# Kernel optimization log

Measured on AMD Instinct MI355X. Metric: run time of the kernel, lower is better.

## Reference

```python
import jax, jax.numpy as jnp
import numpy as np

B, L, M, D, H, FF, W = 2, 2048, 2048, 1024, 16, 4096, 64
DH = D // H


def _layernorm(x, g, b, eps=1e-5):
    mu = x.mean(-1, keepdims=True)
    var = ((x - mu) ** 2).mean(-1, keepdims=True)
    return (x - mu) / jnp.sqrt(var + eps) * g + b


def _mha(qx, kx, wq, bq, wk, bk, wv, bv, wo, bo, mask, bias):
    Bq, Lq, _ = qx.shape
    Lk = kx.shape[1]
    q = (qx @ wq + bq).reshape(Bq, Lq, H, DH).transpose(0, 2, 1, 3)  # [B,H,Lq,DH]
    k = (kx @ wk + bk).reshape(Bq, Lk, H, DH).transpose(0, 2, 1, 3)
    v = (kx @ wv + bv).reshape(Bq, Lk, H, DH).transpose(0, 2, 1, 3)
    s = jnp.einsum('bhqd,bhkd->bhqk', q, k) / jnp.sqrt(jnp.asarray(DH, qx.dtype))
    if bias is not None:
        s = s + bias[None]  # bias: [H,Lq,Lk]
    if mask is not None:
        s = jnp.where(mask[None, None], s, jnp.asarray(-1e9, qx.dtype))
    a = jax.nn.softmax(s, axis=-1)
    o = jnp.einsum('bhqk,bhkd->bhqd', a, v).transpose(0, 2, 1, 3).reshape(Bq, Lq, D)
    return o @ wo + bo


def _forward(x, mem,
             swq, sbq, swk, sbk, swv, sbv, swo, sbo,
             cwq, cbq, cwk, cbk, cwv, cbv, cwo, cbo,
             w1, b1, w2, b2,
             g1, be1, g2, be2, g3, be3):
    i = jnp.arange(L)[:, None]
    j = jnp.arange(L)[None, :]
    # causal local window mask: attend to j<=i with i-j < W
    mask = (j <= i) & ((i - j) < W)
    # ALiBi slopes for power-of-2 head counts: 2^{-8h/H}, h=1..H
    slopes = (2.0 ** (-8.0 * jnp.arange(1, H + 1, dtype=x.dtype) / H))
    bias = slopes[:, None, None] * (j - i).astype(x.dtype)[None]  # [H,L,L], <=0 on causal part
    sa = _mha(x, x, swq, sbq, swk, sbk, swv, sbv, swo, sbo, mask, bias)
    x = _layernorm(x + sa, g1, be1)
    # cross-attn mask is all ones -> no masking, no bias
    ca = _mha(x, mem, cwq, cbq, cwk, cbk, cwv, cbv, cwo, cbo, None, None)
    x = _layernorm(x + ca, g2, be2)
    ff = jax.nn.gelu(x @ w1 + b1, approximate=False) @ w2 + b2
    return _layernorm(x + ff, g3, be3)


def setup_inputs() -> dict:
    key = jax.random.key(0)
    ks = jax.random.split(key, 16)
    s = 0.02
    inp = {
        'x': jax.random.normal(ks[0], (B, L, D), jnp.float32),
        'mem': jax.random.normal(ks[1], (B, M, D), jnp.float32),
    }
    # self-attn params
    for n, k in zip(['swq', 'swk', 'swv', 'swo'], jax.random.split(ks[2], 4)):
        inp[n] = jax.random.normal(k, (D, D), jnp.float32) * s
    for n in ['sbq', 'sbk', 'sbv', 'sbo']:
        inp[n] = jnp.zeros((D,), jnp.float32)
    # cross-attn params
    for n, k in zip(['cwq', 'cwk', 'cwv', 'cwo'], jax.random.split(ks[3], 4)):
        inp[n] = jax.random.normal(k, (D, D), jnp.float32) * s
    for n in ['cbq', 'cbk', 'cbv', 'cbo']:
        inp[n] = jnp.zeros((D,), jnp.float32)
    # FFN params
    inp['w1'] = jax.random.normal(ks[4], (D, FF), jnp.float32) * s
    inp['b1'] = jnp.zeros((FF,), jnp.float32)
    inp['w2'] = jax.random.normal(ks[5], (FF, D), jnp.float32) * s
    inp['b2'] = jnp.zeros((D,), jnp.float32)
    # LayerNorm params
    for n in ['g1', 'g2', 'g3']:
        inp[n] = jnp.ones((D,), jnp.float32)
    for n in ['be1', 'be2', 'be3']:
        inp[n] = jnp.zeros((D,), jnp.float32)
    return inp


def reference(x, mem,
              swq, sbq, swk, sbk, swv, sbv, swo, sbo,
              cwq, cbq, cwk, cbk, cwv, cbv, cwo, cbo,
              w1, b1, w2, b2,
              g1, be1, g2, be2, g3, be3):
    return _forward(x, mem,
                    swq, sbq, swk, sbk, swv, sbv, swo, sbo,
                    cwq, cbq, cwk, cbk, cwv, cbv, cwo, cbo,
                    w1, b1, w2, b2,
                    g1, be1, g2, be2, g3, be3)
```

## Files before the change

kernel.cpp:

```cpp
#include <hip/hip_runtime.h>
#include <hip/hip_bf16.h>
#include <math.h>

#define Bc 2
#define Lc 2048
#define Mc 2048
#define Dc 1024
#define Hc 16
#define FFc 4096
#define DHc 64

typedef __bf16 bf16;
typedef float f32x4 __attribute__((ext_vector_type(4)));
typedef __bf16 bf16x8 __attribute__((ext_vector_type(8)));
typedef __bf16 bf16x4 __attribute__((ext_vector_type(4)));
typedef __bf16 bf16x2 __attribute__((ext_vector_type(2)));

struct Ptrs8 { const float* p[8]; };

__device__ inline void gload16(const bf16* g, const bf16* lds_base) {
  __builtin_amdgcn_global_load_lds(
      (const __attribute__((address_space(1))) void*)g,
      (__attribute__((address_space(3))) void*)lds_base, 16, 0, 0);
}

#define WAIT_VM(n) asm volatile("s_waitcnt vmcnt(" #n ")" ::: "memory")
#define WAIT_LGKM(n) asm volatile("s_waitcnt lgkmcnt(" #n ")" ::: "memory")
#define RAW_BAR() __builtin_amdgcn_s_barrier()
#define SCHED_FENCE() __builtin_amdgcn_sched_barrier(0)

__device__ inline float gelu_f(float v) {
  float u = 0.7978845608f * (v + 0.044715f * v * v * v);
  float e = exp2f(u * 2.885390082f);
  float th = 1.0f - 2.0f / (e + 1.0f);
  return 0.5f * v * (1.0f + th);
}

__device__ inline int xcd_remap(int flat, int nwg) {
  int cpx = nwg >> 3;
  return (flat & 7) * cpx + (flat >> 3);
}

__global__ __launch_bounds__(256) void k_f2b(const float* __restrict__ in,
                                             bf16* __restrict__ out, long n4) {
  long i = (long)blockIdx.x * 256 + threadIdx.x;
  if (i >= n4) return;
  f32x4 v = *(const f32x4*)(in + i * 4);
  bf16x4 o;
  o[0] = (bf16)v[0]; o[1] = (bf16)v[1]; o[2] = (bf16)v[2]; o[3] = (bf16)v[3];
  *(bf16x4*)(out + i * 4) = o;
}

__global__ __launch_bounds__(256) void k_transpose_w8(Ptrs8 srcs,
                                                      bf16* __restrict__ out) {
  __shared__ float tile[64][65];
  const float* in = srcs.p[blockIdx.z];
  bf16* o = out + (long)blockIdx.z * Dc * Dc;
  int n0 = blockIdx.x * 64, k0 = blockIdx.y * 64;
  int t = threadIdx.x;
  int tr = t >> 4, tc = (t & 15) * 4;
#pragma unroll
  for (int p = 0; p < 4; p++) {
    int r = p * 16 + tr;
    f32x4 v = *(const f32x4*)(in + (long)(k0 + r) * Dc + n0 + tc);
    tile[r][tc] = v[0]; tile[r][tc + 1] = v[1];
    tile[r][tc + 2] = v[2]; tile[r][tc + 3] = v[3];
  }
  __syncthreads();
#pragma unroll
  for (int p = 0; p < 4; p++) {
    int rn = p * 16 + tr;
    bf16x4 ov;
    ov[0] = (bf16)tile[tc + 0][rn]; ov[1] = (bf16)tile[tc + 1][rn];
    ov[2] = (bf16)tile[tc + 2][rn]; ov[3] = (bf16)tile[tc + 3][rn];
    *(bf16x4*)(o + (long)(n0 + rn) * Dc + k0 + tc) = ov;
  }
}

__global__ __launch_bounds__(256) void k_transpose_w(const float* __restrict__ in,
                                                     bf16* __restrict__ out,
                                                     int K, int N) {
  __shared__ float tile[64][65];
  int n0 = blockIdx.x * 64, k0 = blockIdx.y * 64;
  int t = threadIdx.x;
  int tr = t >> 4, tc = (t & 15) * 4;
#pragma unroll
  for (int p = 0; p < 4; p++) {
    int r = p * 16 + tr;
    f32x4 v = *(const f32x4*)(in + (long)(k0 + r) * N + n0 + tc);
    tile[r][tc] = v[0]; tile[r][tc + 1] = v[1];
    tile[r][tc + 2] = v[2]; tile[r][tc + 3] = v[3];
  }
  __syncthreads();
#pragma unroll
  for (int p = 0; p < 4; p++) {
    int rn = p * 16 + tr;
    bf16x4 o;
    o[0] = (bf16)tile[tc + 0][rn]; o[1] = (bf16)tile[tc + 1][rn];
    o[2] = (bf16)tile[tc + 2][rn]; o[3] = (bf16)tile[tc + 3][rn];
    *(bf16x4*)(out + (long)(n0 + rn) * K + k0 + tc) = o;
  }
}

__global__ __launch_bounds__(256) void k_transpose_v(const bf16* __restrict__ vb,
                                                     bf16* __restrict__ vt, int N) {
  __shared__ bf16 tile[64][72];
  int j0 = blockIdx.x * 64;
  int bh = blockIdx.y; int b = bh >> 4; int h = bh & 15;
  int t = threadIdx.x;
#pragma unroll
  for (int c = 0; c < 2; c++) {
    int id = t + c * 256;
    int r = id >> 3, c8 = (id & 7) * 8;
    *(bf16x8*)&tile[r][c8] =
        *(const bf16x8*)(vb + ((long)(b * N + j0 + r)) * Dc + h * DHc + c8);
  }
  __syncthreads();
#pragma unroll
  for (int c = 0; c < 2; c++) {
    int id = t + c * 256;
    int d = id >> 3, j8 = (id & 7) * 8;
    bf16x8 o;
#pragma unroll
    for (int e = 0; e < 8; e++) o[e] = tile[j8 + e][d];
    *(bf16x8*)(vt + ((long)bh * DHc + d) * N + j0 + j8) = o;
  }
}

__global__ __launch_bounds__(256) void k_gemm128(
    const bf16* __restrict__ A0, const bf16* __restrict__ A1,
    const bf16* __restrict__ A2, long lda,
    const bf16* __restrict__ B0, long bstride,
    bf16* __restrict__ outB, long ldc, long cstride,
    const float* __restrict__ bias0, const float* __restrict__ bias1,
    const float* __restrict__ bias2, int Kdim, int act, float scale0) {
  __shared__ __align__(16) bf16 As[2][128 * 64];
  __shared__ __align__(16) bf16 Bs[2][128 * 64];
  int gx = gridDim.x, gy = gridDim.y;
  int nwg = gx * gy * gridDim.z;
  int flat = (blockIdx.z * gy + blockIdx.y) * gx + blockIdx.x;
  int f2 = xcd_remap(flat, nwg);
  int bxi = f2 % gx; int tmp = f2 / gx;
  int byi = tmp % gy; int z = tmp / gy;
  const bf16* A = (z == 0) ? A0 : ((z == 1) ? A1 : A2);
  const bf16* Bt = B0 + (long)z * bstride;
  const float* bias = (z == 0) ? bias0 : ((z == 1) ? bias1 : bias2);
  float scl = (z == 0) ? scale0 : 1.0f;
  long cbase = (long)z * cstride;
  int bm = byi * 128, bn = bxi * 128;
  int t = threadIdx.x, w = t >> 6, lane = t & 63;
  int wm = w >> 1, wn = w & 1;
  int lr = lane & 15, lg = lane >> 4;
  int srow = lane >> 3;
  int scol = (((lane & 7) * 16) ^ ((lane >> 3) << 4)) >> 1;
  f32x4 acc[4][4] = {};
  int nk = Kdim >> 6;
  auto stage = [&](int buf, int kt2) {
    long k0 = (long)kt2 * 64;
#pragma unroll
    for (int i = 0; i < 4; i++) {
      int row = (i * 4 + w) * 8 + srow;
      gload16(A + (long)(bm + row) * lda + k0 + scol, &As[buf][(i * 4 + w) * 512]);
      gload16(Bt + (long)(bn + row) * Kdim + k0 + scol, &Bs[buf][(i * 4 + w) * 512]);
    }
  };
  stage(0, 0);
  if (nk > 1) stage(1, 1);
  for (int kt = 0; kt < nk; ++kt) {
    int cur = kt & 1;
    if (kt + 1 < nk) { WAIT_VM(8); } else { WAIT_VM(0); }
    RAW_BAR();
    SCHED_FENCE();
    const char* pa = (const char*)&As[cur][0];
    const char* pb = (const char*)&Bs[cur][0];
    int xr = (lr & 7) << 4;
    bf16x8 af[2][4], bfr[2][4];
#pragma unroll
    for (int m = 0; m < 4; m++) {
      int row = wm * 64 + m * 16 + lr;
      af[0][m] = *(const bf16x8*)(pa + (row << 7) + ((lg * 16) ^ xr));
    }
#pragma unroll
    for (int n = 0; n < 4; n++) {
      int row = wn * 64 + n * 16 + lr;
      bfr[0][n] = *(const bf16x8*)(pb + (row << 7) + ((lg * 16) ^ xr));
    }
    SCHED_FENCE();
#pragma unroll
    for (int m = 0; m < 4; m++) {
      int row = wm * 64 + m * 16 + lr;
      af[1][m] = *(const bf16x8*)(pa + (row << 7) + ((64 + lg * 16) ^ xr));
    }
#pragma unroll
    for (int n = 0; n < 4; n++) {
      int row = wn * 64 + n * 16 + lr;
      bfr[1][n] = *(const bf16x8*)(pb + (row << 7) + ((64 + lg * 16) ^ xr));
    }
    SCHED_FENCE();
    WAIT_LGKM(8);
    SCHED_FENCE();
#pragma unroll
    for (int m = 0; m < 4; m++)
#pragma unroll
      for (int n = 0; n < 4; n++)
        acc[m][n] = __builtin_amdgcn_mfma_f32_16x16x32_bf16(af[0][m], bfr[0][n],
                                                            acc[m][n], 0, 0, 0);
    WAIT_LGKM(0);
    SCHED_FENCE();
    RAW_BAR();
    if (kt + 2 < nk) stage(cur, kt + 2);
    SCHED_FENCE();
#pragma unroll
    for (int m = 0; m < 4; m++)
#pragma unroll
      for (int n = 0; n < 4; n++)
        acc[m][n] = __builtin_amdgcn_mfma_f32_16x16x32_bf16(af[1][m], bfr[1][n],
                                                            acc[m][n], 0, 0, 0);
  }
#pragma unroll
  for (int n = 0; n < 4; n++) {
    int cg = bn + wn * 64 + n * 16 + lr;
    float bv = bias ? bias[cg] : 0.0f;
#pragma unroll
    for (int m = 0; m < 4; m++) {
#pragma unroll
      for (int rr = 0; rr < 4; rr++) {
        int rg = bm + wm * 64 + m * 16 + lg * 4 + rr;
        float v = (acc[m][n][rr] + bv) * scl;
        if (act == 1) v = gelu_f(v);
        outB[cbase + (long)rg * ldc + cg] = (bf16)v;
      }
    }
  }
}

__global__ __launch_bounds__(256) void k_gemmsk(
    const bf16* __restrict__ A, long lda,
    const bf16* __restrict__ Bt, int Kfull,
    bf16* __restrict__ psum, long slab, int Kchunk, int ldc) {
  __shared__ __align__(16) bf16 As[2][128 * 64];
  __shared__ __align__(16) bf16 Bs[2][128 * 64];
  int gx = gridDim.x, gy = gridDim.y;
  int nwg = gx * gy * gridDim.z;
  int flat = (blockIdx.z * gy + blockIdx.y) * gx + blockIdx.x;
  int f2 = xcd_remap(flat, nwg);
  int bxi = f2 % gx; int tmp = f2 / gx;
  int byi = tmp % gy; int z = tmp / gy;
  int bm = byi * 128, bn = bxi * 128;
  int t = threadIdx.x, w = t >> 6, lane = t & 63;
  int wm = w >> 1, wn = w & 1;
  int lr = lane & 15, lg = lane >> 4;
  int srow = lane >> 3;
  int scol = (((lane & 7) * 16) ^ ((lane >> 3) << 4)) >> 1;
  f32x4 acc[4][4] = {};
  int nk = Kchunk >> 6;
  long kstart = (long)z * Kchunk;
  auto stage = [&](int buf, int kt2) {
    long k0 = kstart + (long)kt2 * 64;
#pragma unroll
    for (int i = 0; i < 4; i++) {
      int row = (i * 4 + w) * 8 + srow;
      gload16(A + (long)(bm + row) * lda + k0 + scol, &As[buf][(i * 4 + w) * 512]);
      gload16(Bt + (long)(bn + row) * Kfull + k0 + scol, &Bs[buf][(i * 4 + w) * 512]);
    }
  };
  stage(0, 0);
  if (nk > 1) stage(1, 1);
  for (int kt = 0; kt < nk; ++kt) {
    int cur = kt & 1;
    if (kt + 1 < nk) { WAIT_VM(8); } else { WAIT_VM(0); }
    RAW_BAR();
    SCHED_FENCE();
    const char* pa = (const char*)&As[cur][0];
    const char* pb = (const char*)&Bs[cur][0];
    int xr = (lr & 7) << 4;
    bf16x8 af[2][4], bfr[2][4];
#pragma unroll
    for (int m = 0; m < 4; m++) {
      int row = wm * 64 + m * 16 + lr;
      af[0][m] = *(const bf16x8*)(pa + (row << 7) + ((lg * 16) ^ xr));
    }
#pragma unroll
    for (int n = 0; n < 4; n++) {
      int row = wn * 64 + n * 16 + lr;
      bfr[0][n] = *(const bf16x8*)(pb + (row << 7) + ((lg * 16) ^ xr));
    }
    SCHED_FENCE();
#pragma unroll
    for (int m = 0; m < 4; m++) {
      int row = wm * 64 + m * 16 + lr;
      af[1][m] = *(const bf16x8*)(pa + (row << 7) + ((64 + lg * 16) ^ xr));
    }
#pragma unroll
    for (int n = 0; n < 4; n++) {
      int row = wn * 64 + n * 16 + lr;
      bfr[1][n] = *(const bf16x8*)(pb + (row << 7) + ((64 + lg * 16) ^ xr));
    }
    SCHED_FENCE();
    WAIT_LGKM(8);
    SCHED_FENCE();
#pragma unroll
    for (int m = 0; m < 4; m++)
#pragma unroll
      for (int n = 0; n < 4; n++)
        acc[m][n] = __builtin_amdgcn_mfma_f32_16x16x32_bf16(af[0][m], bfr[0][n],
                                                            acc[m][n], 0, 0, 0);
    WAIT_LGKM(0);
    SCHED_FENCE();
    RAW_BAR();
    if (kt + 2 < nk) stage(cur, kt + 2);
    SCHED_FENCE();
#pragma unroll
    for (int m = 0; m < 4; m++)
#pragma unroll
      for (int n = 0; n < 4; n++)
        acc[m][n] = __builtin_amdgcn_mfma_f32_16x16x32_bf16(af[1][m], bfr[1][n],
                                                            acc[m][n], 0, 0, 0);
  }
  bf16* po = psum + (long)z * slab;
#pragma unroll
  for (int n = 0; n < 4; n++) {
    int cg = bn + wn * 64 + n * 16 + lr;
#pragma unroll
    for (int m = 0; m < 4; m++) {
#pragma unroll
      for (int rr = 0; rr < 4; rr++) {
        int rg = bm + wm * 64 + m * 16 + lg * 4 + rr;
        po[(long)rg * ldc + cg] = (bf16)acc[m][n][rr];
      }
    }
  }
}

template <int WINDOWED>
__global__ __launch_bounds__(256) void k_flash(const bf16* __restrict__ Qg,
                                               const bf16* __restrict__ Kg,
                                               const bf16* __restrict__ Vtg,
                                               bf16* __restrict__ Og, int nkv) {
  __shared__ __align__(16) bf16 Qs[64 * 64];
  __shared__ __align__(16) bf16 Ks[2][64 * 64];
  __shared__ __align__(16) bf16 Vs[2][64 * 64];
  int flat = blockIdx.y * 32 + blockIdx.x;
  int flat2 = (flat & 7) * 128 + (flat >> 3);
  int i0 = (flat2 & 31) * 64;
  int bh = flat2 >> 5;
  int b = bh >> 4, h = bh & 15;
  int t = threadIdx.x, w = t >> 6, lane = t & 63;
  int lr = lane & 15, lg = lane >> 4;
  long qoff = ((long)b * Lc + i0) * Dc + h * DHc;
  long koff = ((long)b * nkv) * Dc + h * DHc;
  long vtoff = (long)bh * DHc * nkv;
  int o0 = w * 1024 + (lane << 4), o1 = o0 + 4096;
  int r0 = o0 >> 7, c0 = (o0 & 127) ^ ((r0 & 7) << 4);
  int r1 = o1 >> 7, c1 = (o1 & 127) ^ ((r1 & 7) << 4);
  int d0 = c0 >> 1, d1 = c1 >> 1;
  gload16(Qg + qoff + (long)r0 * Dc + d0, &Qs[w * 512]);
  gload16(Qg + qoff + (long)r1 * Dc + d1, &Qs[2048 + w * 512]);
  int kb0 = WINDOWED ? (i0 >= 64 ? i0 - 64 : 0) : 0;
  int nt = WINDOWED ? ((i0 - kb0) >> 6) + 1 : (nkv >> 6);
  auto stage = [&](int buf, int kbase) {
    gload16(Kg + koff + (long)(kbase + r0) * Dc + d0, &Ks[buf][w * 512]);
    gload16(Kg + koff + (long)(kbase + r1) * Dc + d1, &Ks[buf][2048 + w * 512]);
    gload16(Vtg + vtoff + (long)r0 * nkv + kbase + d0, &Vs[buf][w * 512]);
    gload16(Vtg + vtoff + (long)r1 * nkv + kbase + d1, &Vs[buf][2048 + w * 512]);
  };
  stage(0, kb0);
  WAIT_VM(4);
  RAW_BAR();
  SCHED_FENCE();
  bf16x8 bq[2];
#pragma unroll
  for (int ks = 0; ks < 2; ks++) {
    int rq = w * 16 + lr, cb = ks * 64 + lg * 16;
    bq[ks] = *(const bf16x8*)&Qs[((rq << 7) + (cb ^ ((rq & 7) << 4))) >> 1];
  }
  char* pbase = (char*)&Qs[w * 1024];
  float mrun = -1e30f, lrun = 0.f;
  float mx_c = 0.0f;
  f32x4 oa[4] = {};
  f32x4 lacc = {};
  bf16x8 ones;
#pragma unroll
  for (int e = 0; e < 8; e++) ones[e] = (bf16)1.0f;
  float slopeL2 = WINDOWED ? exp2f(-0.5f * (float)(h + 1)) * 1.44269504f : 0.0f;
  int qabs = i0 + w * 16 + lr;
  int xr16 = (lr & 7) << 4;
  for (int tch = 0; tch < nt; tch++) {
    int cur = tch & 1;
    if (tch + 1 < nt) {
      stage(cur ^ 1, kb0 + (tch + 1) * 64);
      WAIT_VM(4);
    } else {
      WAIT_VM(0);
    }
    RAW_BAR();
    SCHED_FENCE();
    int kbase = kb0 + tch * 64;
    f32x4 st[4] = {};
    __builtin_amdgcn_s_setprio(1);
#pragma unroll
    for (int ks = 0; ks < 2; ks++) {
#pragma unroll
      for (int m = 0; m < 4; m++) {
        int rk = m * 16 + lr, cb = ks * 64 + lg * 16;
        bf16x8 ka = *(const bf16x8*)&Ks[cur][((rk << 7) + (cb ^ ((rk & 7) << 4))) >> 1];
        st[m] = __builtin_amdgcn_mfma_f32_16x16x32_bf16(ka, bq[ks], st[m], 0, 0, 0);
      }
    }
    __builtin_amdgcn_s_setprio(0);
    if (WINDOWED) {
      float sc[4][4];
#pragma unroll
      for (int m = 0; m < 4; m++)
#pragma unroll
        for (int rr = 0; rr < 4; rr++) {
          float v = st[m][rr];
          int kab = kbase + m * 16 + lg * 4 + rr;
          v += slopeL2 * (float)(kab - qabs);
          bool valid = (kab <= qabs) && (qabs - kab < 64);
          sc[m][rr] = valid ? v : -3.0e38f;
        }
      float pmax = sc[0][0];
#pragma unroll
      for (int m = 0; m < 4; m++)
#pragma unroll
        for (int rr = 0; rr < 4; rr++) pmax = fmaxf(pmax, sc[m][rr]);
      pmax = fmaxf(pmax, __shfl_xor(pmax, 16));
      pmax = fmaxf(pmax, __shfl_xor(pmax, 32));
      float mx = mrun;
      if (!__all(pmax - mrun <= 8.0f)) {
        mx = fmaxf(mrun, pmax);
        float corr = exp2f(mrun - mx);
        mrun = mx;
        lrun *= corr;
        float cq[4];
#pragma unroll
        for (int rr = 0; rr < 4; rr++) cq[rr] = __shfl(corr, lg * 4 + rr);
#pragma unroll
        for (int jd = 0; jd < 4; jd++) {
          oa[jd][0] *= cq[0]; oa[jd][1] *= cq[1];
          oa[jd][2] *= cq[2]; oa[jd][3] *= cq[3];
        }
      }
      float ps = 0.f;
#pragma unroll
      for (int m = 0; m < 4; m++) {
        float p0 = exp2f(sc[m][0] - mx);
        float p1 = exp2f(sc[m][1] - mx);
        float p2 = exp2f(sc[m][2] - mx);
        float p3 = exp2f(sc[m][3] - mx);
        ps += (p0 + p1) + (p2 + p3);
        bf16x4 pw; pw[0] = (bf16)p0; pw[1] = (bf16)p1;
        pw[2] = (bf16)p2; pw[3] = (bf16)p3;
        *(bf16x4*)(pbase + (lr << 7) + ((m * 32 + lg * 8) ^ xr16)) = pw;
      }
      lrun += ps;
      __builtin_amdgcn_s_setprio(1);
#pragma unroll
      for (int ks = 0; ks < 2; ks++) {
        bf16x8 pa = *(const bf16x8*)(pbase + (lr << 7) +
                                     ((ks * 64 + lg * 16) ^ xr16));
#pragma unroll
        for (int jd = 0; jd < 4; jd++) {
          int rv = jd * 16 + lr, cb = ks * 64 + lg * 16;
          bf16x8 vf = *(const bf16x8*)&Vs[cur][((rv << 7) + (cb ^ ((rv & 7) << 4))) >> 1];
          oa[jd] = __builtin_amdgcn_mfma_f32_16x16x32_bf16(pa, vf, oa[jd], 0, 0, 0);
        }
      }
      __builtin_amdgcn_s_setprio(0);
    } else {
      if (tch == 0) {
        float pmax = st[0][0];
#pragma unroll
        for (int m = 0; m < 4; m++)
#pragma unroll
          for (int rr = 0; rr < 4; rr++) pmax = fmaxf(pmax, st[m][rr]);
        pmax = fmaxf(pmax, __shfl_xor(pmax, 16));
        pmax = fmaxf(pmax, __shfl_xor(pmax, 32));
        mx_c = pmax;
      }
#pragma unroll
      for (int m = 0; m < 4; m++) {
        float p0 = exp2f(st[m][0] - mx_c);
        float p1 = exp2f(st[m][1] - mx_c);
        float p2 = exp2f(st[m][2] - mx_c);
        float p3 = exp2f(st[m][3] - mx_c);
        bf16x4 pw; pw[0] = (bf16)p0; pw[1] = (bf16)p1;
        pw[2] = (bf16)p2; pw[3] = (bf16)p3;
        *(bf16x4*)(pbase + (lr << 7) + ((m * 32 + lg * 8) ^ xr16)) = pw;
      }
      __builtin_amdgcn_s_setprio(1);
#pragma unroll
      for (int ks = 0; ks < 2; ks++) {
        bf16x8 pa = *(const bf16x8*)(pbase + (lr << 7) +
                                     ((ks * 64 + lg * 16) ^ xr16));
        lacc = __builtin_amdgcn_mfma_f32_16x16x32_bf16(pa, ones, lacc, 0, 0, 0);
#pragma unroll
        for (int jd = 0; jd < 4; jd++) {
          int rv = jd * 16 + lr, cb = ks * 64 + lg * 16;
          bf16x8 vf = *(const bf16x8*)&Vs[cur][((rv << 7) + (cb ^ ((rv & 7) << 4))) >> 1];
          oa[jd] = __builtin_amdgcn_mfma_f32_16x16x32_bf16(pa, vf, oa[jd], 0, 0, 0);
        }
      }
      __builtin_amdgcn_s_setprio(0);
      float lm = fmaxf(fmaxf(lacc[0], lacc[1]), fmaxf(lacc[2], lacc[3]));
      if (!__all(lm < 16777216.0f)) {
        const float cs = 2.3283064365386963e-10f;
        mx_c += 32.0f;
#pragma unroll
        for (int jd = 0; jd < 4; jd++) {
          oa[jd][0] *= cs; oa[jd][1] *= cs;
          oa[jd][2] *= cs; oa[jd][3] *= cs;
        }
        lacc[0] *= cs; lacc[1] *= cs; lacc[2] *= cs; lacc[3] *= cs;
      }
    }
    WAIT_LGKM(0);
    SCHED_FENCE();
    RAW_BAR();
  }
  if (WINDOWED) {
    float ls = lrun + __shfl_xor(lrun, 16);
    ls += __shfl_xor(ls, 32);
    float inv = 1.0f / ls;
    float iq[4];
#pragma unroll
    for (int rr = 0; rr < 4; rr++) iq[rr] = __shfl(inv, lg * 4 + rr);
#pragma unroll
    for (int rr = 0; rr < 4; rr++) {
      int qo = i0 + w * 16 + lg * 4 + rr;
#pragma unroll
      for (int jd = 0; jd < 4; jd++)
        Og[((long)b * Lc + qo) * Dc + h * DHc + jd * 16 + lr] =
            (bf16)(oa[jd][rr] * iq[rr]);
    }
  } else {
#pragma unroll
    for (int rr = 0; rr < 4; rr++) {
      float inv = 1.0f / lacc[rr];
      int qo = i0 + w * 16 + lg * 4 + rr;
#pragma unroll
      for (int jd = 0; jd < 4; jd++)
        Og[((long)b * Lc + qo) * Dc + h * DHc + jd * 16 + lr] =
            (bf16)(oa[jd][rr] * inv);
    }
  }
}

template <int NS>
__global__ __launch_bounds__(256) void k_lnred(const bf16* __restrict__ psum,
                                               long slab,
                                               const float* __restrict__ bias,
                                               const float* __restrict__ addsrc,
                                               const float* __restrict__ g,
                                               const float* __restrict__ bb,
                                               float* __restrict__ outF,
                                               bf16* __restrict__ outB) {
  long row = blockIdx.x;
  int t = threadIdx.x; int lane = t & 63; int wid = t >> 6;
  __shared__ float red[8];
  bf16x4 v0 = *(const bf16x4*)(psum + row * Dc + t * 4);
  float v[4] = {(float)v0[0], (float)v0[1], (float)v0[2], (float)v0[3]};
#pragma unroll
  for (int s = 1; s < NS; s++) {
    bf16x4 u = *(const bf16x4*)(psum + s * slab + row * Dc + t * 4);
    v[0] += (float)u[0]; v[1] += (float)u[1];
    v[2] += (float)u[2]; v[3] += (float)u[3];
  }
  f32x4 bv = *(const f32x4*)(bias + t * 4);
  f32x4 av = *(const f32x4*)(addsrc + row * Dc + t * 4);
  v[0] += bv[0] + av[0]; v[1] += bv[1] + av[1];
  v[2] += bv[2] + av[2]; v[3] += bv[3] + av[3];
  float s = v[0] + v[1] + v[2] + v[3];
  float s2 = v[0] * v[0] + v[1] * v[1] + v[2] * v[2] + v[3] * v[3];
#pragma unroll
  for (int off = 1; off < 64; off <<= 1) {
    s += __shfl_xor(s, off);
    s2 += __shfl_xor(s2, off);
  }
  if (lane == 0) { red[wid] = s; red[4 + wid] = s2; }
  __syncthreads();
  s = red[0] + red[1] + red[2] + red[3];
  s2 = red[4] + red[5] + red[6] + red[7];
  float mu = s * (1.0f / Dc);
  float var = s2 * (1.0f / Dc) - mu * mu;
  float rs = rsqrtf(var + 1e-5f);
#pragma unroll
  for (int e = 0; e < 4; e++) {
    int c = t * 4 + e;
    float y = (v[e] - mu) * rs * g[c] + bb[c];
    if (outF) outF[row * Dc + c] = y;
    if (outB) outB[row * Dc + c] = (bf16)y;
  }
}

extern "C" void kernel_launch(void* const* d_in, const int* in_sizes, int n_in,
                              void* d_out, int out_size, void* d_ws,
                              size_t ws_size, hipStream_t stream) {
  (void)in_sizes; (void)n_in; (void)out_size; (void)ws_size;
  const float* x = (const float*)d_in[0];
  const float* mem = (const float*)d_in[1];
  const float* swq = (const float*)d_in[2];
  const float* swk = (const float*)d_in[3];
  const float* swv = (const float*)d_in[4];
  const float* swo = (const float*)d_in[5];
  const float* sbq = (const float*)d_in[6];
  const float* sbk = (const float*)d_in[7];
  const float* sbv = (const float*)d_in[8];
  const float* sbo = (const float*)d_in[9];
  const float* cwq = (const float*)d_in[10];
  const float* cwk = (const float*)d_in[11];
  const float* cwv = (const float*)d_in[12];
  const float* cwo = (const float*)d_in[13];
  const float* cbq = (const float*)d_in[14];
  const float* cbk = (const float*)d_in[15];
  const float* cbv = (const float*)d_in[16];
  const float* cbo = (const float*)d_in[17];
  const float* w1 = (const float*)d_in[18];
  const float* b1 = (const float*)d_in[19];
  const float* w2 = (const float*)d_in[20];
  const float* b2 = (const float*)d_in[21];
  const float* g1 = (const float*)d_in[22];
  const float* g2 = (const float*)d_in[23];
  const float* g3 = (const float*)d_in[24];
  const float* be1 = (const float*)d_in[25];
  const float* be2 = (const float*)d_in[26];
  const float* be3 = (const float*)d_in[27];
  float* out = (float*)d_out;

  char* ws = (char*)d_ws;
  size_t off = 0;
  auto alloc = [&](size_t bytes) -> char* {
    char* p = ws + off;
    off = (off + bytes + 255) & ~(size_t)255;
    return p;
  };

  const long BL = (long)Bc * Lc;
  const long BM = (long)Bc * Mc;
  const long DD = (long)Dc * Dc;
  const long SL = BL * Dc;
  const float QSCL = 0.125f * 1.44269504f;

  bf16* wT0 = (bf16*)alloc((size_t)8 * DD * 2);
  bf16* w1T = (bf16*)alloc((size_t)FFc * Dc * 2);
  bf16* w2T = (bf16*)alloc((size_t)Dc * FFc * 2);
  bf16* xb = (bf16*)alloc((size_t)BL * Dc * 2);
  bf16* memb = (bf16*)alloc((size_t)BM * Dc * 2);
  bf16* x1b = (bf16*)alloc((size_t)BL * Dc * 2);
  bf16* x2b = (bf16*)alloc((size_t)BL * Dc * 2);
  bf16* qb = (bf16*)alloc((size_t)BL * Dc * 2);
  bf16* kb = (bf16*)alloc((size_t)BM * Dc * 2);
  bf16* vb = (bf16*)alloc((size_t)BM * Dc * 2);
  bf16* ob = (bf16*)alloc((size_t)BL * Dc * 2);
  bf16* vtS = (bf16*)alloc((size_t)Bc * Hc * DHc * Lc * 2);
  bf16* vtC = (bf16*)alloc((size_t)Bc * Hc * DHc * Mc * 2);
  float* x1f = (float*)alloc((size_t)BL * Dc * 4);
  float* x2f = (float*)alloc((size_t)BL * Dc * 4);
  bf16* ffh = (bf16*)alloc((size_t)BL * FFc * 2);
  bf16* psum = (bf16*)alloc((size_t)4 * SL * 2);

  Ptrs8 srcs;
  srcs.p[0] = swq; srcs.p[1] = swk; srcs.p[2] = swv; srcs.p[3] = swo;
  srcs.p[4] = cwq; srcs.p[5] = cwk; srcs.p[6] = cwv; srcs.p[7] = cwo;
  k_transpose_w8<<<dim3(Dc / 64, Dc / 64, 8), 256, 0, stream>>>(srcs, wT0);
  k_transpose_w<<<dim3(FFc / 64, Dc / 64), 256, 0, stream>>>(w1, w1T, Dc, FFc);
  k_transpose_w<<<dim3(Dc / 64, FFc / 64), 256, 0, stream>>>(w2, w2T, FFc, Dc);
  k_f2b<<<dim3((unsigned)(BL * Dc / 4 / 256)), 256, 0, stream>>>(x, xb, BL * Dc / 4);
  k_f2b<<<dim3((unsigned)(BM * Dc / 4 / 256)), 256, 0, stream>>>(mem, memb, BM * Dc / 4);

  k_gemm128<<<dim3(Dc / 128, BL / 128, 3), 256, 0, stream>>>(
      xb, xb, xb, Dc, wT0, DD, qb, Dc, SL, sbq, sbk, sbv, Dc, 0, QSCL);
  k_transpose_v<<<dim3(Lc / 64, Bc * Hc), 256, 0, stream>>>(vb, vtS, Lc);
  k_flash<1><<<dim3(Lc / 64, Bc * Hc), 256, 0, stream>>>(qb, kb, vtS, ob, Lc);
  k_gemmsk<<<dim3(Dc / 128, BL / 128, 2), 256, 0, stream>>>(
      ob, Dc, wT0 + 3 * DD, Dc, psum, SL, 512, Dc);
  k_lnred<2><<<dim3((unsigned)BL), 256, 0, stream>>>(psum, SL, sbo, x, g1, be1,
                                                     x1f, x1b);

  k_gemm128<<<dim3(Dc / 128, BM / 128, 3), 256, 0, stream>>>(
      x1b, memb, memb, Dc, wT0 + 4 * DD, DD, qb, Dc, SL, cbq, cbk, cbv, Dc, 0, QSCL);
  k_transpose_v<<<dim3(Mc / 64, Bc * Hc), 256, 0, stream>>>(vb, vtC, Mc);
  k_flash<0><<<dim3(Lc / 64, Bc * Hc), 256, 0, stream>>>(qb, kb, vtC, ob, Mc);
  k_gemmsk<<<dim3(Dc / 128, BL / 128, 2), 256, 0, stream>>>(
      ob, Dc, wT0 + 7 * DD, Dc, psum, SL, 512, Dc);
  k_lnred<2><<<dim3((unsigned)BL), 256, 0, stream>>>(psum, SL, cbo, x1f, g2, be2,
                                                     x2f, x2b);

  k_gemm128<<<dim3(FFc / 128, BL / 128, 1), 256, 0, stream>>>(
      x2b, x2b, x2b, Dc, w1T, 0, ffh, FFc, 0, b1, b1, b1, Dc, 1, 1.0f);
  k_gemmsk<<<dim3(Dc / 128, BL / 128, 4), 256, 0, stream>>>(
      ffh, FFc, w2T, FFc, psum, SL, 1024, Dc);
  k_lnred<4><<<dim3((unsigned)BL), 256, 0, stream>>>(psum, SL, b2, x2f, g3, be3,
                                                     out, nullptr);
}
```

Measured before the change: 359.9 us.

## Split flash kernel; cross-attention processes 128 queries per block, add MFMA priority in GEMMs

The templated flash kernel is split into a self-attention version and a cross-attention version. The cross-attention kernel now handles 128 query rows per workgroup, 32 per wave, so each K/V tile staged into shared memory is reused by twice as many queries, halving K/V global traffic and the grid size. The Q buffer is reused as the per-wave P scratch. Separately, the GEMM kernels raise wave priority around the MFMA blocks. The trade-offs are more registers per wave, which may lower occupancy, and fewer workgroups to fill the GPU.

Result: no change. 363.6 us, median of 2 (+1.0%).

```diff
diff --git a/kernel.cpp b/kernel.cpp
--- a/kernel.cpp
+++ b/kernel.cpp
@@ -199,23 +199,27 @@
     SCHED_FENCE();
     WAIT_LGKM(8);
     SCHED_FENCE();
+    __builtin_amdgcn_s_setprio(1);
 #pragma unroll
     for (int m = 0; m < 4; m++)
 #pragma unroll
       for (int n = 0; n < 4; n++)
         acc[m][n] = __builtin_amdgcn_mfma_f32_16x16x32_bf16(af[0][m], bfr[0][n],
                                                             acc[m][n], 0, 0, 0);
+    __builtin_amdgcn_s_setprio(0);
     WAIT_LGKM(0);
     SCHED_FENCE();
     RAW_BAR();
     if (kt + 2 < nk) stage(cur, kt + 2);
     SCHED_FENCE();
+    __builtin_amdgcn_s_setprio(1);
 #pragma unroll
     for (int m = 0; m < 4; m++)
 #pragma unroll
       for (int n = 0; n < 4; n++)
         acc[m][n] = __builtin_amdgcn_mfma_f32_16x16x32_bf16(af[1][m], bfr[1][n],
                                                             acc[m][n], 0, 0, 0);
+    __builtin_amdgcn_s_setprio(0);
   }
 #pragma unroll
   for (int n = 0; n < 4; n++) {
@@ -299,23 +303,27 @@
     SCHED_FENCE();
     WAIT_LGKM(8);
     SCHED_FENCE();
+    __builtin_amdgcn_s_setprio(1);
 #pragma unroll
     for (int m = 0; m < 4; m++)
 #pragma unroll
       for (int n = 0; n < 4; n++)
         acc[m][n] = __builtin_amdgcn_mfma_f32_16x16x32_bf16(af[0][m], bfr[0][n],
                                                             acc[m][n], 0, 0, 0);
+    __builtin_amdgcn_s_setprio(0);
     WAIT_LGKM(0);
     SCHED_FENCE();
     RAW_BAR();
     if (kt + 2 < nk) stage(cur, kt + 2);
     SCHED_FENCE();
+    __builtin_amdgcn_s_setprio(1);
 #pragma unroll
     for (int m = 0; m < 4; m++)
 #pragma unroll
       for (int n = 0; n < 4; n++)
         acc[m][n] = __builtin_amdgcn_mfma_f32_16x16x32_bf16(af[1][m], bfr[1][n],
                                                             acc[m][n], 0, 0, 0);
+    __builtin_amdgcn_s_setprio(0);
   }
   bf16* po = psum + (long)z * slab;
 #pragma unroll
@@ -332,11 +340,10 @@
   }
 }
 
-template <int WINDOWED>
-__global__ __launch_bounds__(256) void k_flash(const bf16* __restrict__ Qg,
-                                               const bf16* __restrict__ Kg,
-                                               const bf16* __restrict__ Vtg,
-                                               bf16* __restrict__ Og, int nkv) {
+__global__ __launch_bounds__(256) void k_flash_self(const bf16* __restrict__ Qg,
+                                                    const bf16* __restrict__ Kg,
+                                                    const bf16* __restrict__ Vtg,
+                                                    bf16* __restrict__ Og, int nkv) {
   __shared__ __align__(16) bf16 Qs[64 * 64];
   __shared__ __align__(16) bf16 Ks[2][64 * 64];
   __shared__ __align__(16) bf16 Vs[2][64 * 64];
@@ -356,8 +363,8 @@
   int d0 = c0 >> 1, d1 = c1 >> 1;
   gload16(Qg + qoff + (long)r0 * Dc + d0, &Qs[w * 512]);
   gload16(Qg + qoff + (long)r1 * Dc + d1, &Qs[2048 + w * 512]);
-  int kb0 = WINDOWED ? (i0 >= 64 ? i0 - 64 : 0) : 0;
-  int nt = WINDOWED ? ((i0 - kb0) >> 6) + 1 : (nkv >> 6);
+  int kb0 = i0 >= 64 ? i0 - 64 : 0;
+  int nt = ((i0 - kb0) >> 6) + 1;
   auto stage = [&](int buf, int kbase) {
     gload16(Kg + koff + (long)(kbase + r0) * Dc + d0, &Ks[buf][w * 512]);
     gload16(Kg + koff + (long)(kbase + r1) * Dc + d1, &Ks[buf][2048 + w * 512]);
@@ -376,13 +383,8 @@
   }
   char* pbase = (char*)&Qs[w * 1024];
   float mrun = -1e30f, lrun = 0.f;
-  float mx_c = 0.0f;
   f32x4 oa[4] = {};
-  f32x4 lacc = {};
-  bf16x8 ones;
-#pragma unroll
-  for (int e = 0; e < 8; e++) ones[e] = (bf16)1.0f;
-  float slopeL2 = WINDOWED ? exp2f(-0.5f * (float)(h + 1)) * 1.44269504f : 0.0f;
+  float slopeL2 = exp2f(-0.5f * (float)(h + 1)) * 1.44269504f;
   int qabs = i0 + w * 16 + lr;
   int xr16 = (lr & 7) << 4;
   for (int tch = 0; tch < nt; tch++) {
@@ -408,143 +410,241 @@
       }
     }
     __builtin_amdgcn_s_setprio(0);
-    if (WINDOWED) {
-      float sc[4][4];
-#pragma unroll
-      for (int m = 0; m < 4; m++)
-#pragma unroll
-        for (int rr = 0; rr < 4; rr++) {
-          float v = st[m][rr];
-          int kab = kbase + m * 16 + lg * 4 + rr;
-          v += slopeL2 * (float)(kab - qabs);
-          bool valid = (kab <= qabs) && (qabs - kab < 64);
-          sc[m][rr] = valid ? v : -3.0e38f;
-        }
-      float pmax = sc[0][0];
-#pragma unroll
-      for (int m = 0; m < 4; m++)
-#pragma unroll
-        for (int rr = 0; rr < 4; rr++) pmax = fmaxf(pmax, sc[m][rr]);
+    float sc[4][4];
+#pragma unroll
+    for (int m = 0; m < 4; m++)
+#pragma unroll
+      for (int rr = 0; rr < 4; rr++) {
+        float v = st[m][rr];
+        int kab = kbase + m * 16 + lg * 4 + rr;
+        v += slopeL2 * (float)(kab - qabs);
+        bool valid = (kab <= qabs) && (qabs - kab < 64);
+        sc[m][rr] = valid ? v : -3.0e38f;
+      }
+    float pmax = sc[0][0];
+#pragma unroll
+    for (int m = 0; m < 4; m++)
+#pragma unroll
+      for (int rr = 0; rr < 4; rr++) pmax = fmaxf(pmax, sc[m][rr]);
+    pmax = fmaxf(pmax, __shfl_xor(pmax, 16));
+    pmax = fmaxf(pmax, __shfl_xor(pmax, 32));
+    float mx = mrun;
+    if (!__all(pmax - mrun <= 8.0f)) {
+      mx = fmaxf(mrun, pmax);
+      float corr = exp2f(mrun - mx);
+      mrun = mx;
+      lrun *= corr;
+      float cq[4];
+#pragma unroll
+      for (int rr = 0; rr < 4; rr++) cq[rr] = __shfl(corr, lg * 4 + rr);
+#pragma unroll
+      for (int jd = 0; jd < 4; jd++) {
+        oa[jd][0] *= cq[0]; oa[jd][1] *= cq[1];
+        oa[jd][2] *= cq[2]; oa[jd][3] *= cq[3];
+      }
+    }
+    float ps = 0.f;
+#pragma unroll
+    for (int m = 0; m < 4; m++) {
+      float p0 = exp2f(sc[m][0] - mx);
+      float p1 = exp2f(sc[m][1] - mx);
+      float p2 = exp2f(sc[m][2] - mx);
+      float p3 = exp2f(sc[m][3] - mx);
+      ps += (p0 + p1) + (p2 + p3);
+      bf16x4 pw; pw[0] = (bf16)p0; pw[1] = (bf16)p1;
+      pw[2] = (bf16)p2; pw[3] = (bf16)p3;
+      *(bf16x4*)(pbase + (lr << 7) + ((m * 32 + lg * 8) ^ xr16)) = pw;
+    }
+    lrun += ps;
+    __builtin_amdgcn_s_setprio(1);
+#pragma unroll
+    for (int ks = 0; ks < 2; ks++) {
+      bf16x8 pa = *(const bf16x8*)(pbase + (lr << 7) +
+                                   ((ks * 64 + lg * 16) ^ xr16));
+#pragma unroll
+      for (int jd = 0; jd < 4; jd++) {
+        int rv = jd * 16 + lr, cb = ks * 64 + lg * 16;
+        bf16x8 vf = *(const bf16x8*)&Vs[cur][((rv << 7) + (cb ^ ((rv & 7) << 4))) >> 1];
+        oa[jd] = __builtin_amdgcn_mfma_f32_16x16x32_bf16(pa, vf, oa[jd], 0, 0, 0);
+      }
+    }
+    __builtin_amdgcn_s_setprio(0);
+    WAIT_LGKM(0);
+    SCHED_FENCE();
+    RAW_BAR();
+  }
+  float ls = lrun + __shfl_xor(lrun, 16);
+  ls += __shfl_xor(ls, 32);
+  float inv = 1.0f / ls;
+  float iq[4];
+#pragma unroll
+  for (int rr = 0; rr < 4; rr++) iq[rr] = __shfl(inv, lg * 4 + rr);
+#pragma unroll
+  for (int rr = 0; rr < 4; rr++) {
+    int qo = i0 + w * 16 + lg * 4 + rr;
+#pragma unroll
+    for (int jd = 0; jd < 4; jd++)
+      Og[((long)b * Lc + qo) * Dc + h * DHc + jd * 16 + lr] =
+          (bf16)(oa[jd][rr] * iq[rr]);
+  }
+}
+
+__global__ __launch_bounds__(256) void k_flash_cross(const bf16* __restrict__ Qg,
+                                                     const bf16* __restrict__ Kg,
+                                                     const bf16* __restrict__ Vtg,
+                                                     bf16* __restrict__ Og,
+                                                     int nkv) {
+  __shared__ __align__(16) bf16 QP[128 * 64];
+  __shared__ __align__(16) bf16 Ks[2][64 * 64];
+  __shared__ __align__(16) bf16 Vs[2][64 * 64];
+  int gx = gridDim.x;
+  int nwg = gx * gridDim.y;
+  int flat = blockIdx.y * gx + blockIdx.x;
+  int f2 = (flat & 7) * (nwg >> 3) + (flat >> 3);
+  int i0 = (f2 % gx) * 128;
+  int bh = f2 / gx;
+  int b = bh >> 4, h = bh & 15;
+  int t = threadIdx.x, w = t >> 6, lane = t & 63;
+  int lr = lane & 15, lg = lane >> 4;
+  long qoff = ((long)b * Lc + i0) * Dc + h * DHc;
+  long koff = ((long)b * nkv) * Dc + h * DHc;
+  long vtoff = (long)bh * DHc * nkv;
+  int o0 = w * 1024 + (lane << 4), o1 = o0 + 4096;
+  int r0 = o0 >> 7, c0 = (o0 & 127) ^ ((r0 & 7) << 4);
+  int r1 = o1 >> 7, c1 = (o1 & 127) ^ ((r1 & 7) << 4);
+  int d0 = c0 >> 1, d1 = c1 >> 1;
+#pragma unroll
+  for (int i = 0; i < 4; i++) {
+    int oq = (i * 4 + w) * 1024 + (lane << 4);
+    int rq = oq >> 7;
+    int cq = (oq & 127) ^ ((rq & 7) << 4);
+    gload16(Qg + qoff + (long)rq * Dc + (cq >> 1), &QP[(i * 4 + w) * 512]);
+  }
+  auto stage = [&](int buf, int kbase) {
+    gload16(Kg + koff + (long)(kbase + r0) * Dc + d0, &Ks[buf][w * 512]);
+    gload16(Kg + koff + (long)(kbase + r1) * Dc + d1, &Ks[buf][2048 + w * 512]);
+    gload16(Vtg + vtoff + (long)r0 * nkv + kbase + d0, &Vs[buf][w * 512]);
+    gload16(Vtg + vtoff + (long)r1 * nkv + kbase + d1, &Vs[buf][2048 + w * 512]);
+  };
+  stage(0, 0);
+  WAIT_VM(4);
+  RAW_BAR();
+  SCHED_FENCE();
+  bf16x8 bq[2][2];
+#pragma unroll
+  for (int qg = 0; qg < 2; qg++)
+#pragma unroll
+    for (int ks = 0; ks < 2; ks++) {
+      int rq = w * 32 + qg * 16 + lr, cb = ks * 64 + lg * 16;
+      bq[qg][ks] = *(const bf16x8*)((const char*)QP + (rq << 7) + (cb ^ ((rq & 7) << 4)));
+    }
+  float mx_c = 0.0f;
+  f32x4 oa[2][4] = {};
+  f32x4 lacc[2] = {};
+  bf16x8 ones;
+#pragma unroll
+  for (int e = 0; e < 8; e++) ones[e] = (bf16)1.0f;
+  int xr16 = (lr & 7) << 4;
+  char* pb0 = (char*)QP + w * 4096;
+  char* pb1 = (char*)QP + w * 4096 + 2048;
+  int nt = nkv >> 6;
+  for (int tch = 0; tch < nt; tch++) {
+    int cur = tch & 1;
+    if (tch + 1 < nt) {
+      stage(cur ^ 1, (tch + 1) * 64);
+      WAIT_VM(4);
+    } else {
+      WAIT_VM(0);
+    }
+    RAW_BAR();
+    SCHED_FENCE();
+    f32x4 st[2][4] = {};
+    __builtin_amdgcn_s_setprio(1);
+#pragma unroll
+    for (int ks = 0; ks < 2; ks++) {
+#pragma unroll
+      for (int m = 0; m < 4; m++) {
+        int rk = m * 16 + lr, cb = ks * 64 + lg * 16;
+        bf16x8 ka = *(const bf16x8*)&Ks[cur][((rk << 7) + (cb ^ ((rk & 7) << 4))) >> 1];
+        st[0][m] = __builtin_amdgcn_mfma_f32_16x16x32_bf16(ka, bq[0][ks], st[0][m], 0, 0, 0);
+        st[1][m] = __builtin_amdgcn_mfma_f32_16x16x32_bf16(ka, bq[1][ks], st[1][m], 0, 0, 0);
+      }
+    }
+    __builtin_amdgcn_s_setprio(0);
+    if (tch == 0) {
+      float pmax = st[0][0][0];
+#pragma unroll
+      for (int qg = 0; qg < 2; qg++)
+#pragma unroll
+        for (int m = 0; m < 4; m++)
+#pragma unroll
+          for (int rr = 0; rr < 4; rr++) pmax = fmaxf(pmax, st[qg][m][rr]);
       pmax = fmaxf(pmax, __shfl_xor(pmax, 16));
       pmax = fmaxf(pmax, __shfl_xor(pmax, 32));
-      float mx = mrun;
-      if (!__all(pmax - mrun <= 8.0f)) {
-        mx = fmaxf(mrun, pmax);
-        float corr = exp2f(mrun - mx);
-        mrun = mx;
-        lrun *= corr;
-        float cq[4];
-#pragma unroll
-        for (int rr = 0; rr < 4; rr++) cq[rr] = __shfl(corr, lg * 4 + rr);
-#pragma unroll
-        for (int jd = 0; jd < 4; jd++) {
-          oa[jd][0] *= cq[0]; oa[jd][1] *= cq[1];
-          oa[jd][2] *= cq[2]; oa[jd][3] *= cq[3];
-        }
-      }
-      float ps = 0.f;
+      mx_c = pmax;
+    }
+#pragma unroll
+    for (int qg = 0; qg < 2; qg++) {
+      char* pbq = qg ? pb1 : pb0;
 #pragma unroll
       for (int m = 0; m < 4; m++) {
-        float p0 = exp2f(sc[m][0] - mx);
-        float p1 = exp2f(sc[m][1] - mx);
-        float p2 = exp2f(sc[m][2] - mx);
-        float p3 = exp2f(sc[m][3] - mx);
-        ps += (p0 + p1) + (p2 + p3);
+        float p0 = exp2f(st[qg][m][0] - mx_c);
+        float p1 = exp2f(st[qg][m][1] - mx_c);
+        float p2 = exp2f(st[qg][m][2] - mx_c);
+        float p3 = exp2f(st[qg][m][3] - mx_c);
         bf16x4 pw; pw[0] = (bf16)p0; pw[1] = (bf16)p1;
         pw[2] = (bf16)p2; pw[3] = (bf16)p3;
-        *(bf16x4*)(pbase + (lr << 7) + ((m * 32 + lg * 8) ^ xr16)) = pw;
-      }
-      lrun += ps;
-      __builtin_amdgcn_s_setprio(1);
-#pragma unroll
-      for (int ks = 0; ks < 2; ks++) {
-        bf16x8 pa = *(const bf16x8*)(pbase + (lr << 7) +
-                                     ((ks * 64 + lg * 16) ^ xr16));
+        *(bf16x4*)(pbq + (lr << 7) + ((m * 32 + lg * 8) ^ xr16)) = pw;
+      }
+    }
+    __builtin_amdgcn_s_setprio(1);
+#pragma unroll
+    for (int ks = 0; ks < 2; ks++) {
+      int cb = ks * 64 + lg * 16;
+      bf16x8 pa0 = *(const bf16x8*)(pb0 + (lr << 7) + (cb ^ xr16));
+      bf16x8 pa1 = *(const bf16x8*)(pb1 + (lr << 7) + (cb ^ xr16));
+      lacc[0] = __builtin_amdgcn_mfma_f32_16x16x32_bf16(pa0, ones, lacc[0], 0, 0, 0);
+      lacc[1] = __builtin_amdgcn_mfma_f32_16x16x32_bf16(pa1, ones, lacc[1], 0, 0, 0);
+#pragma unroll
+      for (int jd = 0; jd < 4; jd++) {
+        int rv = jd * 16 + lr;
+        bf16x8 vf = *(const bf16x8*)&Vs[cur][((rv << 7) + (cb ^ ((rv & 7) << 4))) >> 1];
+        oa[0][jd] = __builtin_amdgcn_mfma_f32_16x16x32_bf16(pa0, vf, oa[0][jd], 0, 0, 0);
+        oa[1][jd] = __builtin_amdgcn_mfma_f32_16x16x32_bf16(pa1, vf, oa[1][jd], 0, 0, 0);
+      }
+    }
+    __builtin_amdgcn_s_setprio(0);
+    float lm = fmaxf(fmaxf(lacc[0][0], lacc[0][1]), fmaxf(lacc[0][2], lacc[0][3]));
+    lm = fmaxf(lm, fmaxf(fmaxf(lacc[1][0], lacc[1][1]), fmaxf(lacc[1][2], lacc[1][3])));
+    if (!__all(lm < 16777216.0f)) {
+      const float cs = 2.3283064365386963e-10f;
+      mx_c += 32.0f;
+#pragma unroll
+      for (int qg = 0; qg < 2; qg++) {
 #pragma unroll
         for (int jd = 0; jd < 4; jd++) {
-          int rv = jd * 16 + lr, cb = ks * 64 + lg * 16;
-          bf16x8 vf = *(const bf16x8*)&Vs[cur][((rv << 7) + (cb ^ ((rv & 7) << 4))) >> 1];
-          oa[jd] = __builtin_amdgcn_mfma_f32_16x16x32_bf16(pa, vf, oa[jd], 0, 0, 0);
+          oa[qg][jd][0] *= cs; oa[qg][jd][1] *= cs;
+          oa[qg][jd][2] *= cs; oa[qg][jd][3] *= cs;
         }
-      }
-      __builtin_amdgcn_s_setprio(0);
-    } else {
-      if (tch == 0) {
-        float pmax = st[0][0];
-#pragma unroll
-        for (int m = 0; m < 4; m++)
-#pragma unroll
-          for (int rr = 0; rr < 4; rr++) pmax = fmaxf(pmax, st[m][rr]);
-        pmax = fmaxf(pmax, __shfl_xor(pmax, 16));
-        pmax = fmaxf(pmax, __shfl_xor(pmax, 32));
-        mx_c = pmax;
-      }
-#pragma unroll
-      for (int m = 0; m < 4; m++) {
-        float p0 = exp2f(st[m][0] - mx_c);
-        float p1 = exp2f(st[m][1] - mx_c);
-        float p2 = exp2f(st[m][2] - mx_c);
-        float p3 = exp2f(st[m][3] - mx_c);
-        bf16x4 pw; pw[0] = (bf16)p0; pw[1] = (bf16)p1;
-        pw[2] = (bf16)p2; pw[3] = (bf16)p3;
-        *(bf16x4*)(pbase + (lr << 7) + ((m * 32 + lg * 8) ^ xr16)) = pw;
-      }
-      __builtin_amdgcn_s_setprio(1);
-#pragma unroll
-      for (int ks = 0; ks < 2; ks++) {
-        bf16x8 pa = *(const bf16x8*)(pbase + (lr << 7) +
-                                     ((ks * 64 + lg * 16) ^ xr16));
-        lacc = __builtin_amdgcn_mfma_f32_16x16x32_bf16(pa, ones, lacc, 0, 0, 0);
-#pragma unroll
-        for (int jd = 0; jd < 4; jd++) {
-          int rv = jd * 16 + lr, cb = ks * 64 + lg * 16;
-          bf16x8 vf = *(const bf16x8*)&Vs[cur][((rv << 7) + (cb ^ ((rv & 7) << 4))) >> 1];
-          oa[jd] = __builtin_amdgcn_mfma_f32_16x16x32_bf16(pa, vf, oa[jd], 0, 0, 0);
-        }
-      }
-      __builtin_amdgcn_s_setprio(0);
-      float lm = fmaxf(fmaxf(lacc[0], lacc[1]), fmaxf(lacc[2], lacc[3]));
-      if (!__all(lm < 16777216.0f)) {
-        const float cs = 2.3283064365386963e-10f;
-        mx_c += 32.0f;
-#pragma unroll
-        for (int jd = 0; jd < 4; jd++) {
-          oa[jd][0] *= cs; oa[jd][1] *= cs;
-          oa[jd][2] *= cs; oa[jd][3] *= cs;
-        }
-        lacc[0] *= cs; lacc[1] *= cs; lacc[2] *= cs; lacc[3] *= cs;
+        lacc[qg][0] *= cs; lacc[qg][1] *= cs;
+        lacc[qg][2] *= cs; lacc[qg][3] *= cs;
       }
     }
     WAIT_LGKM(0);
     SCHED_FENCE();
     RAW_BAR();
   }
-  if (WINDOWED) {
-    float ls = lrun + __shfl_xor(lrun, 16);
-    ls += __shfl_xor(ls, 32);
-    float inv = 1.0f / ls;
-    float iq[4];
-#pragma unroll
-    for (int rr = 0; rr < 4; rr++) iq[rr] = __shfl(inv, lg * 4 + rr);
+#pragma unroll
+  for (int qg = 0; qg < 2; qg++)
 #pragma unroll
     for (int rr = 0; rr < 4; rr++) {
-      int qo = i0 + w * 16 + lg * 4 + rr;
+      float inv = 1.0f / lacc[qg][rr];
+      int qo = i0 + w * 32 + qg * 16 + lg * 4 + rr;
 #pragma unroll
       for (int jd = 0; jd < 4; jd++)
         Og[((long)b * Lc + qo) * Dc + h * DHc + jd * 16 + lr] =
-            (bf16)(oa[jd][rr] * iq[rr]);
-    }
-  } else {
-#pragma unroll
-    for (int rr = 0; rr < 4; rr++) {
-      float inv = 1.0f / lacc[rr];
-      int qo = i0 + w * 16 + lg * 4 + rr;
-#pragma unroll
-      for (int jd = 0; jd < 4; jd++)
-        Og[((long)b * Lc + qo) * Dc + h * DHc + jd * 16 + lr] =
-            (bf16)(oa[jd][rr] * inv);
-    }
-  }
+            (bf16)(oa[qg][jd][rr] * inv);
+    }
 }
 
 template <int NS>
@@ -672,7 +772,7 @@
   k_gemm128<<<dim3(Dc / 128, BL / 128, 3), 256, 0, stream>>>(
       xb, xb, xb, Dc, wT0, DD, qb, Dc, SL, sbq, sbk, sbv, Dc, 0, QSCL);
   k_transpose_v<<<dim3(Lc / 64, Bc * Hc), 256, 0, stream>>>(vb, vtS, Lc);
-  k_flash<1><<<dim3(Lc / 64, Bc * Hc), 256, 0, stream>>>(qb, kb, vtS, ob, Lc);
+  k_flash_self<<<dim3(Lc / 64, Bc * Hc), 256, 0, stream>>>(qb, kb, vtS, ob, Lc);
   k_gemmsk<<<dim3(Dc / 128, BL / 128, 2), 256, 0, stream>>>(
       ob, Dc, wT0 + 3 * DD, Dc, psum, SL, 512, Dc);
   k_lnred<2><<<dim3((unsigned)BL), 256, 0, stream>>>(psum, SL, sbo, x, g1, be1,
@@ -681,7 +781,7 @@
   k_gemm128<<<dim3(Dc / 128, BM / 128, 3), 256, 0, stream>>>(
       x1b, memb, memb, Dc, wT0 + 4 * DD, DD, qb, Dc, SL, cbq, cbk, cbv, Dc, 0, QSCL);
   k_transpose_v<<<dim3(Mc / 64, Bc * Hc), 256, 0, stream>>>(vb, vtC, Mc);
-  k_flash<0><<<dim3(Lc / 64, Bc * Hc), 256, 0, stream>>>(qb, kb, vtC, ob, Mc);
+  k_flash_cross<<<dim3(Lc / 128, Bc * Hc), 256, 0, stream>>>(qb, kb, vtC, ob, Mc);
   k_gemmsk<<<dim3(Dc / 128, BL / 128, 2), 256, 0, stream>>>(
       ob, Dc, wT0 + 7 * DD, Dc, psum, SL, 512, Dc);
   k_lnred<2><<<dim3((unsigned)BL), 256, 0, stream>>>(psum, SL, cbo, x1f, g2, be2,
```
